# Optimization experiments

Hardware: AMD Instinct MI355X
Metric: run time of the kernel (lower is better)

Reference implementation:

```python
import jax, jax.numpy as jnp
import numpy as np

N_NODES = 100000
N_EDGES = 50000
NNZ = 400000          # 8 node slots per hyperedge, each node in exactly 4 hyperedges
IN_CH = 64            # ONE_HOT_0_ENCODING_SIZE
HID = 256
ALPHA = -1.5          # HNHN edge-cardinality exponent
BETA = -0.5           # HNHN node-cardinality exponent


def setup_inputs() -> dict:
    key = jax.random.key(0)
    ks = jax.random.split(key, 12)
    x_0 = jax.random.normal(ks[0], (N_NODES, IN_CH), dtype=jnp.float32)
    # COO incidence: every node appears NNZ//N_NODES times, every edge has NNZ//N_EDGES members
    rows = jax.random.permutation(
        ks[1], jnp.tile(jnp.arange(N_NODES, dtype=jnp.int32), NNZ // N_NODES))
    cols = jnp.repeat(jnp.arange(N_EDGES, dtype=jnp.int32), NNZ // N_EDGES)
    vals = jnp.ones((NNZ,), dtype=jnp.float32)

    def glorot(k, fi, fo):
        return jax.random.normal(k, (fi, fo), dtype=jnp.float32) * (2.0 / (fi + fo)) ** 0.5

    W0_l0 = glorot(ks[2], IN_CH, HID)
    W1_l0 = glorot(ks[3], HID, HID)
    W0_l1 = glorot(ks[4], HID, HID)
    W1_l1 = glorot(ks[5], HID, HID)
    b1_l0 = jax.random.normal(ks[6], (1, HID), dtype=jnp.float32) * 0.05
    b0_l0 = jax.random.normal(ks[7], (1, HID), dtype=jnp.float32) * 0.05
    b1_l1 = jax.random.normal(ks[8], (1, HID), dtype=jnp.float32) * 0.05
    b0_l1 = jax.random.normal(ks[9], (1, HID), dtype=jnp.float32) * 0.05
    lin_w = glorot(ks[10], HID, 1)
    lin_b = jnp.zeros((1,), dtype=jnp.float32)
    return dict(x_0=x_0, vals=vals, rows=rows, cols=cols,
                W0_l0=W0_l0, W1_l0=W1_l0, b1_l0=b1_l0, b0_l0=b0_l0,
                W0_l1=W0_l1, W1_l1=W1_l1, b1_l1=b1_l1, b0_l1=b0_l1,
                lin_w=lin_w, lin_b=lin_b)


def _normalized_vals(vals, rows, cols):
    """HNHN normalization of the incidence matrix B (n_nodes x n_edges).

    vals_n[k] : entry of  D0_left^{-1} B D1_right(|e|^alpha)        (edge->node)
    vals_t[k] : entry of (D1_left^{-1} B^T D0_right(d(v)^beta))^T   (node->edge)
    """
    seg = jax.ops.segment_sum
    edge_card = seg(vals, cols, num_segments=N_EDGES) ** ALPHA   # |e|^alpha
    node_card = seg(vals, rows, num_segments=N_NODES) ** BETA    # d(v)^beta
    nz = (vals != 0).astype(vals.dtype)                          # nonzero pattern
    d0_inv = 1.0 / seg(edge_card[cols] * nz, rows, num_segments=N_NODES)
    d1_inv = 1.0 / seg(node_card[rows] * nz, cols, num_segments=N_EDGES)
    vals_n = d0_inv[rows] * vals * edge_card[cols]
    vals_t = d1_inv[cols] * vals * node_card[rows]
    return vals_n, vals_t


def _hnhn_layer(x0, rows, cols, vals_n, vals_t, W0, W1, b1, b0):
    # node -> hyperedge: x_1 = relu(B_t_norm^T (x0 W0) + b1)
    m = (x0 @ W0)[rows] * vals_t[:, None]                 # [nnz, HID]
    x1 = jax.nn.relu(jax.ops.segment_sum(m, cols, num_segments=N_EDGES) + b1)
    # hyperedge -> node: x_0 = relu(B_norm (x1 W1) + b0)
    m = (x1 @ W1)[cols] * vals_n[:, None]                 # [nnz, HID]
    x0 = jax.nn.relu(jax.ops.segment_sum(m, rows, num_segments=N_NODES) + b0)
    return x0, x1


def reference(x_0, vals, rows, cols,
              W0_l0, W1_l0, b1_l0, b0_l0,
              W0_l1, W1_l1, b1_l1, b0_l1,
              lin_w, lin_b):
    vals_n, vals_t = _normalized_vals(vals, rows, cols)
    x0, _ = _hnhn_layer(x_0, rows, cols, vals_n, vals_t, W0_l0, W1_l0, b1_l0, b0_l0)
    x0, _ = _hnhn_layer(x0, rows, cols, vals_n, vals_t, W0_l1, W1_l1, b1_l1, b0_l1)
    pooled = jnp.max(x0, axis=0)                          # [HID]
    return pooled @ lin_w + lin_b                         # [1]
```

## Files before the change

kernel.cpp:

```cpp
#include <hip/hip_runtime.h>

#define N_NODES 100000
#define N_EDGES 50000
#define NNZ_    400000
#define MP 100032
#define EP 50048
#define NBN 98
#define NBE 49
#define PRED_ROWS 6250

typedef unsigned short ushort_t;
typedef unsigned int uint_t;

typedef __attribute__((ext_vector_type(8))) short bf16x8;
typedef __attribute__((ext_vector_type(4))) float f32x4;

__device__ __forceinline__ float b2f(ushort_t u) {
    return __uint_as_float(((uint_t)u) << 16);
}
__device__ __forceinline__ ushort_t f2b(float f) {
    uint_t x = __float_as_uint(f);
    uint_t r = (x + 0x7fffu + ((x >> 16) & 1u)) >> 16;
    return (ushort_t)r;
}
__device__ __forceinline__ float ldval(const void* p, int k, int bf) {
    return bf ? b2f(((const ushort_t*)p)[k]) : ((const float*)p)[k];
}
__device__ __forceinline__ float vb(bf16x8 v, int j) {
    return __uint_as_float(((uint_t)(ushort_t)v[j]) << 16);
}

__global__ void k_sentinel(void* out) { ((uint_t*)out)[0] = 0x44894489u; }

__global__ void k_zero(uint_t* p, size_t n) {
    size_t i = (size_t)blockIdx.x * 256 + threadIdx.x;
    size_t stride = (size_t)gridDim.x * 256;
    for (; i < n; i += stride) p[i] = 0u;
}

__global__ void k_checkfill(const void* __restrict__ vals, const int* __restrict__ rows,
                            const int* __restrict__ cols, int* ncntA, int* nidx,
                            int* flags) {
    int k = blockIdx.x * 256 + threadIdx.x;
    int bf = (((const uint_t*)vals)[0] == 0x3F803F80u);
    if (k == 0 && blockIdx.x == 0) flags[0] = bf;
    if (k >= NNZ_) return;
    int bad = 0;
    if (cols[k] != (k >> 3)) bad = 1;
    if (bf) { if (((const ushort_t*)vals)[k] != 0x3F80) bad = 1; }
    else    { if (((const uint_t*)vals)[k] != 0x3F800000u) bad = 1; }
    if (bad) atomicOr(&flags[2], 1);
    int r = rows[k];
    if ((unsigned)r >= (unsigned)N_NODES) { atomicOr(&flags[3], 1); return; }
    int slot = atomicAdd(&ncntA[r], 1);
    if (slot < 4) nidx[r * 4 + slot] = k;
    else atomicOr(&flags[3], 1);
}

__global__ void k_cvt_all(const void* x0, const void* W0l0, const void* W1l0,
                          const void* W0l1, const void* W1l1,
                          const void* b1l0, const void* b0l0, const void* b1l1,
                          const void* b0l1, const void* lw, const void* lb,
                          ushort_t* x0c, ushort_t* Wt0_l0, ushort_t* Wt1_l0,
                          ushort_t* Wt0_l1, ushort_t* Wt1_l1,
                          float* smallf, const int* __restrict__ flags) {
    int bf = flags[0];
    long i = (long)blockIdx.x * 256 + threadIdx.x;
    const long R0V = (long)N_NODES * 64 / 8;
    if (i < R0V) {
        if (!bf) {
            const float* s = (const float*)x0 + i * 8;
            bf16x8 o;
#pragma unroll
            for (int j = 0; j < 8; ++j) o[j] = (short)f2b(s[j]);
            *(bf16x8*)(x0c + i * 8) = o;
        }
        return;
    }
    i -= R0V;
    if (i < 64 * 256) {
        int kk = i >> 8, n = i & 255;
        Wt0_l0[n * 64 + kk] = bf ? ((const ushort_t*)W0l0)[i] : f2b(((const float*)W0l0)[i]);
        return;
    }
    i -= 64 * 256;
    if (i < 65536) {
        int kk = i >> 8, n = i & 255;
        Wt1_l0[n * 256 + kk] = bf ? ((const ushort_t*)W1l0)[i] : f2b(((const float*)W1l0)[i]);
        return;
    }
    i -= 65536;
    if (i < 65536) {
        int kk = i >> 8, n = i & 255;
        Wt0_l1[n * 256 + kk] = bf ? ((const ushort_t*)W0l1)[i] : f2b(((const float*)W0l1)[i]);
        return;
    }
    i -= 65536;
    if (i < 65536) {
        int kk = i >> 8, n = i & 255;
        Wt1_l1[n * 256 + kk] = bf ? ((const ushort_t*)W1l1)[i] : f2b(((const float*)W1l1)[i]);
        return;
    }
    i -= 65536;
    if (i < 1536) {
        int b = i >> 8, t = i & 255;
        const void* srcs[6] = {b1l0, b0l0, b1l1, b0l1, lw, lb};
        int sz = (b == 5) ? 1 : 256;
        if (t < sz) smallf[b * 256 + t] = ldval(srcs[b], t, bf);
    }
}

__global__ void k_hist(const void* __restrict__ vals, const int* __restrict__ rows,
                       const int* __restrict__ cols, int* node_cnt, int* edge_cnt,
                       float* node_delta, float* edge_delta, const int* __restrict__ flags) {
    if ((flags[2] | flags[3]) == 0) return;
    int k = blockIdx.x * 256 + threadIdx.x;
    if (k >= NNZ_) return;
    int r = rows[k], c = cols[k];
    atomicAdd(&node_cnt[r], 1);
    atomicAdd(&edge_cnt[c], 1);
    float v = ldval(vals, k, flags[0]);
    if (v != 1.0f) {
        atomicAdd(&node_delta[r], v - 1.0f);
        atomicAdd(&edge_delta[c], v - 1.0f);
    }
}

__global__ void k_pow(const int* node_cnt, const int* edge_cnt,
                      const float* node_delta, const float* edge_delta,
                      float* node_card, float* edge_card, const int* __restrict__ flags) {
    if ((flags[2] | flags[3]) == 0) return;
    int i = blockIdx.x * 256 + threadIdx.x;
    if (i < N_NODES) {
        float s = (float)node_cnt[i] + node_delta[i];
        node_card[i] = rsqrtf(s);
    }
    if (i < N_EDGES) {
        float s = (float)edge_cnt[i] + edge_delta[i];
        edge_card[i] = 1.0f / (s * sqrtf(s));
    }
}

__global__ void k_dsum(const void* __restrict__ vals, const int* __restrict__ rows,
                       const int* __restrict__ cols, const float* __restrict__ node_card,
                       const float* __restrict__ edge_card, float* d0, float* d1,
                       const int* __restrict__ flags) {
    if ((flags[2] | flags[3]) == 0) return;
    int t = blockIdx.x * 256 + threadIdx.x;
    if (flags[2] == 0) {
        if (t < N_EDGES) {
            const int* rp = rows + t * 8;
            float s = 0.f;
#pragma unroll
            for (int j = 0; j < 8; ++j) s += node_card[rp[j]];
            d1[t] = s;
        }
        if (t < N_NODES) d0[t] = (float)0;
    }
    if (t < NNZ_) {
        float v = ldval(vals, t, flags[0]);
        if (v != 0.0f) {
            int r = rows[t], c = cols[t];
            atomicAdd(&d0[r], edge_card[c]);
            if (flags[2] != 0) atomicAdd(&d1[c], node_card[r]);
        }
    }
}

__global__ void k_scan1(const int* __restrict__ ncnt, const int* __restrict__ ecnt,
                        int* __restrict__ nptr, int* __restrict__ eptr,
                        int* __restrict__ bsumN, int* __restrict__ bsumE,
                        const int* __restrict__ flags) {
    if ((flags[2] | flags[3]) == 0) return;
    __shared__ int s[256];
    int b = blockIdx.x;
    const int* cnt; int* ptr; int* bsum; int n;
    if (b < NBN) { cnt = ncnt; ptr = nptr; bsum = bsumN; n = N_NODES; }
    else { b -= NBN; cnt = ecnt; ptr = eptr; bsum = bsumE; n = N_EDGES; }
    int t = threadIdx.x;
    int base = b * 1024 + t * 4;
    int c0 = 0, c1 = 0, c2 = 0, c3 = 0;
    if (base + 0 < n) c0 = cnt[base + 0];
    if (base + 1 < n) c1 = cnt[base + 1];
    if (base + 2 < n) c2 = cnt[base + 2];
    if (base + 3 < n) c3 = cnt[base + 3];
    int s4 = c0 + c1 + c2 + c3;
    s[t] = s4;
    __syncthreads();
    for (int d = 1; d < 256; d <<= 1) {
        int v = (t >= d) ? s[t - d] : 0;
        __syncthreads();
        s[t] += v;
        __syncthreads();
    }
    int ex = s[t] - s4;
    if (base + 0 < n) ptr[base + 0] = ex;
    if (base + 1 < n) ptr[base + 1] = ex + c0;
    if (base + 2 < n) ptr[base + 2] = ex + c0 + c1;
    if (base + 3 < n) ptr[base + 3] = ex + c0 + c1 + c2;
    if (t == 255) bsum[b] = s[255];
}

__global__ void k_scan2(int* __restrict__ bsumN, int* __restrict__ bsumE,
                        int* __restrict__ nptr, int* __restrict__ eptr,
                        const int* __restrict__ flags) {
    if ((flags[2] | flags[3]) == 0) return;
    __shared__ int s[256];
    int* bsum; int nb; int* tot;
    if (blockIdx.x == 0) { bsum = bsumN; nb = NBN; tot = nptr + N_NODES; }
    else { bsum = bsumE; nb = NBE; tot = eptr + N_EDGES; }
    int t = threadIdx.x;
    int v = (t < nb) ? bsum[t] : 0;
    s[t] = v;
    __syncthreads();
    for (int d = 1; d < 256; d <<= 1) {
        int x = (t >= d) ? s[t - d] : 0;
        __syncthreads();
        s[t] += x;
        __syncthreads();
    }
    if (t < nb) bsum[t] = s[t] - v;
    if (t == 255) *tot = s[255];
}

__global__ void k_scan3(int* __restrict__ nptr, int* __restrict__ eptr,
                        const int* __restrict__ bsumN, const int* __restrict__ bsumE,
                        int* __restrict__ ncnt, int* __restrict__ ecnt,
                        int* __restrict__ ndeg, const int* __restrict__ flags) {
    if ((flags[2] | flags[3]) == 0) return;
    int b = blockIdx.x;
    if (b < 391) {
        int i = b * 256 + threadIdx.x;
        if (i < N_NODES) { nptr[i] += bsumN[i >> 10]; ndeg[i] = ncnt[i]; ncnt[i] = 0; }
    } else {
        int i = (b - 391) * 256 + threadIdx.x;
        if (i < N_EDGES) { eptr[i] += bsumE[i >> 10]; ecnt[i] = 0; }
    }
}

__global__ void k_fill(const int* __restrict__ rows, const int* __restrict__ cols,
                       const int* __restrict__ nptr, const int* __restrict__ eptr,
                       int* ncnt, int* ecnt, int* nidx, int* eidx,
                       const int* __restrict__ flags) {
    if ((flags[2] | flags[3]) == 0) return;
    int k = blockIdx.x * 256 + threadIdx.x;
    if (k >= NNZ_) return;
    int r = rows[k], c = cols[k];
    int pos = nptr[r] + atomicAdd(&ncnt[r], 1);
    nidx[pos] = k;
    int pe = eptr[c] + atomicAdd(&ecnt[c], 1);
    eidx[pe] = k;
}

__global__ void k_pairs(const void* __restrict__ vals, const int* __restrict__ rows,
                        const int* __restrict__ cols,
                        const int* __restrict__ nidx, const int* __restrict__ eidx,
                        const int* __restrict__ ndeg, const float* __restrict__ node_card,
                        const float* __restrict__ edge_card,
                        const float* __restrict__ d0, const float* __restrict__ d1,
                        int2* __restrict__ pairN, int2* __restrict__ pairE,
                        const int* __restrict__ flags) {
    if ((flags[2] | flags[3]) == 0) return;
    int i = blockIdx.x * 256 + threadIdx.x;
    if (i >= NNZ_) return;
    int bf = flags[0];
    int k = nidx[i];
    int r = rows[k], c = cols[k];
    float wn;
    if (flags[2] == 0) wn = (1.0f / (float)ndeg[r]);
    else               wn = ldval(vals, k, bf) * edge_card[c] / d0[r];
    pairN[i] = make_int2(c, __float_as_int(wn));
    int ke = eidx[i];
    int rr = rows[ke];
    float wt = ldval(vals, ke, bf) * node_card[rr] / d1[cols[ke]];
    pairE[i] = make_int2(rr, __float_as_int(wt));
}

template <int K>
__global__ __launch_bounds__(256) void k_gemm2(const ushort_t* __restrict__ A,
                                               const ushort_t* __restrict__ Wt,
                                               ushort_t* __restrict__ C,
                                               const float* __restrict__ bias,
                                               int do_relu) {
    __shared__ ushort_t lds[32 * 512];
    const int tid = threadIdx.x;
    const int lane = tid & 63;
    const int wave = tid >> 6;
    const int r16 = lane & 15;
    const int quad = lane >> 4;
    const int nh = blockIdx.x & 1;
    const int mblk = blockIdx.x >> 1;
    const int nbase = nh * 128;
    const int mbase = mblk * 64 + wave * 16;
    const ushort_t* Arow = A + (size_t)(mbase + r16) * K;

    f32x4 acc[8];
#pragma unroll
    for (int t = 0; t < 8; ++t) acc[t] = (f32x4){0.f, 0.f, 0.f, 0.f};

    constexpr int KCH = (K < 128) ? K : 128;
    constexpr int NF = (KCH / 32) * 8;
    for (int kc = 0; kc < K; kc += KCH) {
        __syncthreads();
        for (int f = wave; f < NF; f += 4) {
            int kb = f >> 3, t = f & 7;
            int n = nbase + t * 16 + r16;
            int kg = kc + kb * 32 + quad * 8;
            *(bf16x8*)(&lds[f * 512 + lane * 8]) = *(const bf16x8*)(Wt + (size_t)n * K + kg);
        }
        __syncthreads();
#pragma unroll
        for (int k0 = 0; k0 < KCH; k0 += 32) {
            bf16x8 af = *(const bf16x8*)(Arow + kc + k0 + quad * 8);
#pragma unroll
            for (int t = 0; t < 8; ++t) {
                bf16x8 bfr = *(const bf16x8*)(&lds[((k0 >> 5) * 8 + t) * 512 + lane * 8]);
                acc[t] = __builtin_amdgcn_mfma_f32_16x16x32_bf16(af, bfr, acc[t], 0, 0, 0);
            }
        }
    }
    const int mo = mbase + quad * 4;
#pragma unroll
    for (int t = 0; t < 8; ++t) {
        int n = nbase + t * 16 + r16;
        float b = bias ? bias[n] : 0.f;
#pragma unroll
        for (int r = 0; r < 4; ++r) {
            float v = acc[t][r] + b;
            if (do_relu) v = fmaxf(v, 0.f);
            C[(size_t)(mo + r) * 256 + n] = f2b(v);
        }
    }
}

template <int C>
__global__ __launch_bounds__(256) void k_aggE(const ushort_t* __restrict__ srcA,
                                              const ushort_t* __restrict__ srcB,
                                              const int* __restrict__ rows,
                                              const int* __restrict__ eptr,
                                              const int2* __restrict__ pairE,
                                              ushort_t* __restrict__ dst,
                                              const int* __restrict__ flags) {
    constexpr int TPS = C / 8;
    constexpr int SPB = 256 / TPS;
    const int sub = threadIdx.x / TPS;
    const int ch8 = (threadIdx.x % TPS) * 8;
    const int segA = blockIdx.x * (2 * SPB) + sub;
    const int segB = segA + SPB;
    const ushort_t* src = flags[0] ? srcA : srcB;
    const int sA = min(segA, N_EDGES - 1), sB = min(segB, N_EDGES - 1);
    float accA[8], accB[8];
    if ((flags[2] | flags[3]) == 0) {
        int4 a0 = *(const int4*)(rows + sA * 8);
        int4 a1 = *(const int4*)(rows + sA * 8 + 4);
        int4 b0 = *(const int4*)(rows + sB * 8);
        int4 b1 = *(const int4*)(rows + sB * 8 + 4);
        bf16x8 va0 = *(const bf16x8*)(src + (size_t)a0.x * C + ch8);
        bf16x8 va1 = *(const bf16x8*)(src + (size_t)a0.y * C + ch8);
        bf16x8 va2 = *(const bf16x8*)(src + (size_t)a0.z * C + ch8);
        bf16x8 va3 = *(const bf16x8*)(src + (size_t)a0.w * C + ch8);
        bf16x8 va4 = *(const bf16x8*)(src + (size_t)a1.x * C + ch8);
        bf16x8 va5 = *(const bf16x8*)(src + (size_t)a1.y * C + ch8);
        bf16x8 va6 = *(const bf16x8*)(src + (size_t)a1.z * C + ch8);
        bf16x8 va7 = *(const bf16x8*)(src + (size_t)a1.w * C + ch8);
        bf16x8 vb0 = *(const bf16x8*)(src + (size_t)b0.x * C + ch8);
        bf16x8 vb1 = *(const bf16x8*)(src + (size_t)b0.y * C + ch8);
        bf16x8 vb2 = *(const bf16x8*)(src + (size_t)b0.z * C + ch8);
        bf16x8 vb3 = *(const bf16x8*)(src + (size_t)b0.w * C + ch8);
        bf16x8 vb4 = *(const bf16x8*)(src + (size_t)b1.x * C + ch8);
        bf16x8 vb5 = *(const bf16x8*)(src + (size_t)b1.y * C + ch8);
        bf16x8 vb6 = *(const bf16x8*)(src + (size_t)b1.z * C + ch8);
        bf16x8 vb7 = *(const bf16x8*)(src + (size_t)b1.w * C + ch8);
#pragma unroll
        for (int j = 0; j < 8; ++j) {
            accA[j] = 0.125f * (((vb(va0,j) + vb(va1,j)) + (vb(va2,j) + vb(va3,j))) +
                                ((vb(va4,j) + vb(va5,j)) + (vb(va6,j) + vb(va7,j))));
            accB[j] = 0.125f * (((vb(vb0,j) + vb(vb1,j)) + (vb(vb2,j) + vb(vb3,j))) +
                                ((vb(vb4,j) + vb(vb5,j)) + (vb(vb6,j) + vb(vb7,j))));
        }
    } else {
        float* accs[2] = {accA, accB};
        int segs[2] = {sA, sB};
        for (int p = 0; p < 2; ++p) {
            float* a = accs[p];
#pragma unroll
            for (int j = 0; j < 8; ++j) a[j] = 0.f;
            int lo = eptr[segs[p]], hi = eptr[segs[p] + 1];
            for (int i = lo; i < hi; ++i) {
                int2 pr = pairE[i];
                float w = __int_as_float(pr.y);
                bf16x8 v = *(const bf16x8*)(src + (size_t)pr.x * C + ch8);
#pragma unroll
                for (int j = 0; j < 8; ++j) a[j] += w * vb(v, j);
            }
        }
    }
    bf16x8 oA, oB;
#pragma unroll
    for (int j = 0; j < 8; ++j) { oA[j] = (short)f2b(accA[j]); oB[j] = (short)f2b(accB[j]); }
    if (segA < N_EDGES) *(bf16x8*)(dst + (size_t)segA * C + ch8) = oA;
    if (segB < N_EDGES) *(bf16x8*)(dst + (size_t)segB * C + ch8) = oB;
}

template <int POOL>
__global__ __launch_bounds__(256) void k_aggN(const ushort_t* __restrict__ src,
                                              const int* __restrict__ nidx,
                                              const int* __restrict__ nptr,
                                              const int2* __restrict__ pairN,
                                              const float* __restrict__ bias,
                                              ushort_t* __restrict__ dst,
                                              float* __restrict__ partial,
                                              const int* __restrict__ flags) {
    __shared__ float sm[8][256];
    const int tid = threadIdx.x;
    const int sub = tid >> 5;
    const int ch8 = (tid & 31) * 8;
    const int segA = blockIdx.x * 16 + sub;
    const int segB = segA + 8;
    float accA[8], accB[8];
    if ((flags[2] | flags[3]) == 0) {
        int4 iA = *(const int4*)(nidx + segA * 4);
        int4 iB = *(const int4*)(nidx + segB * 4);
        bf16x8 vA0 = *(const bf16x8*)(src + (size_t)(iA.x >> 3) * 256 + ch8);
        bf16x8 vA1 = *(const bf16x8*)(src + (size_t)(iA.y >> 3) * 256 + ch8);
        bf16x8 vA2 = *(const bf16x8*)(src + (size_t)(iA.z >> 3) * 256 + ch8);
        bf16x8 vA3 = *(const bf16x8*)(src + (size_t)(iA.w >> 3) * 256 + ch8);
        bf16x8 vB0 = *(const bf16x8*)(src + (size_t)(iB.x >> 3) * 256 + ch8);
        bf16x8 vB1 = *(const bf16x8*)(src + (size_t)(iB.y >> 3) * 256 + ch8);
        bf16x8 vB2 = *(const bf16x8*)(src + (size_t)(iB.z >> 3) * 256 + ch8);
        bf16x8 vB3 = *(const bf16x8*)(src + (size_t)(iB.w >> 3) * 256 + ch8);
#pragma unroll
        for (int j = 0; j < 8; ++j) {
            accA[j] = 0.25f * ((vb(vA0,j) + vb(vA1,j)) + (vb(vA2,j) + vb(vA3,j)));
            accB[j] = 0.25f * ((vb(vB0,j) + vb(vB1,j)) + (vb(vB2,j) + vb(vB3,j)));
        }
    } else {
        float* accs[2] = {accA, accB};
        int segs[2] = {segA, segB};
        for (int p = 0; p < 2; ++p) {
            float* a = accs[p];
#pragma unroll
            for (int j = 0; j < 8; ++j) a[j] = 0.f;
            int lo = nptr[segs[p]], hi = nptr[segs[p] + 1];
            for (int i = lo; i < hi; ++i) {
                int2 pr = pairN[i];
                float w = __int_as_float(pr.y);
                bf16x8 v = *(const bf16x8*)(src + (size_t)pr.x * 256 + ch8);
#pragma unroll
                for (int j = 0; j < 8; ++j) a[j] += w * vb(v, j);
            }
        }
    }
    if (POOL) {
#pragma unroll
        for (int j = 0; j < 8; ++j) {
            float rA = fmaxf(accA[j] + bias[ch8 + j], 0.f);
            float rB = fmaxf(accB[j] + bias[ch8 + j], 0.f);
            sm[sub][ch8 + j] = fmaxf(rA, rB);
        }
        __syncthreads();
        float mm = sm[0][tid];
#pragma unroll
        for (int g = 1; g < 8; ++g) mm = fmaxf(mm, sm[g][tid]);
        partial[(size_t)blockIdx.x * 256 + tid] = mm;
    } else {
        bf16x8 oA, oB;
#pragma unroll
        for (int j = 0; j < 8; ++j) {
            oA[j] = (short)f2b(fmaxf(accA[j] + bias[ch8 + j], 0.f));
            oB[j] = (short)f2b(fmaxf(accB[j] + bias[ch8 + j], 0.f));
        }
        *(bf16x8*)(dst + (size_t)segA * 256 + ch8) = oA;
        *(bf16x8*)(dst + (size_t)segB * 256 + ch8) = oB;
    }
}

__global__ void k_pred(const float* __restrict__ partial, float* pooled) {
    int ch = threadIdx.x;
    float m = 0.f;
    for (int r = blockIdx.x; r < PRED_ROWS; r += gridDim.x)
        m = fmaxf(m, partial[(size_t)r * 256 + ch]);
    atomicMax((int*)&pooled[ch], __float_as_int(m));
}

__global__ void k_final(const float* __restrict__ pooled, const float* __restrict__ smallf,
                        void* out, const int* __restrict__ flags) {
    __shared__ float red[256];
    int c = threadIdx.x;
    red[c] = pooled[c] * smallf[4 * 256 + c];
    __syncthreads();
    for (int s = 128; s > 0; s >>= 1) {
        if (c < s) red[c] += red[c + s];
        __syncthreads();
    }
    if (c == 0) {
        float r = red[0] + smallf[5 * 256 + 0];
        if (flags[0]) ((ushort_t*)out)[0] = f2b(r);
        else          ((float*)out)[0] = r;
    }
}

extern "C" void kernel_launch(void* const* d_in, const int* in_sizes, int n_in,
                              void* d_out, int out_size, void* d_ws, size_t ws_size,
                              hipStream_t stream) {
    const void* x0_in = d_in[0];
    const void* vals  = d_in[1];
    const int* rows = (const int*)d_in[2];
    const int* cols = (const int*)d_in[3];
    const void* W0_l0 = d_in[4];
    const void* W1_l0 = d_in[5];
    const void* b1_l0 = d_in[6];
    const void* b0_l0 = d_in[7];
    const void* W0_l1 = d_in[8];
    const void* W1_l1 = d_in[9];
    const void* b1_l1 = d_in[10];
    const void* b0_l1 = d_in[11];
    const void* lin_w = d_in[12];
    const void* lin_b = d_in[13];

    char* ws = (char*)d_ws;
    size_t off = 0;
    auto alloc = [&](size_t bytes) { size_t o = off; off += (bytes + 255) & ~(size_t)255; return o; };

    size_t o_ncntA      = alloc(MP * 4);
    size_t o_node_cnt   = alloc(MP * 4);
    size_t o_edge_cnt   = alloc(EP * 4);
    size_t o_node_delta = alloc(MP * 4);
    size_t o_edge_delta = alloc(EP * 4);
    size_t o_d0         = alloc(MP * 4);
    size_t o_d1         = alloc(EP * 4);
    size_t o_pooled     = alloc(256 * 4);
    size_t o_flags      = alloc(256);
    size_t zero_end     = off;
    size_t o_ndeg      = alloc(MP * 4);
    size_t o_node_card = alloc(MP * 4);
    size_t o_edge_card = alloc(EP * 4);
    size_t o_node_ptr = alloc((size_t)(MP + 1) * 4);
    size_t o_edge_ptr = alloc((size_t)(EP + 1) * 4);
    size_t o_node_idx = alloc((size_t)NNZ_ * 4);
    size_t o_edge_idx = alloc((size_t)NNZ_ * 4);
    size_t o_bsumN    = alloc(512);
    size_t o_bsumE    = alloc(512);
    size_t o_smallf   = alloc(6 * 256 * 4);
    size_t o_pairN    = alloc((size_t)NNZ_ * 8);
    size_t o_pairE    = alloc((size_t)NNZ_ * 8);
    size_t o_Wt0_l0 = alloc(256 * 64 * 2);
    size_t o_Wt1_l0 = alloc(256 * 256 * 2);
    size_t o_Wt0_l1 = alloc(256 * 256 * 2);
    size_t o_Wt1_l1 = alloc(256 * 256 * 2);
    size_t o_E1 = alloc((size_t)EP * 256 * 2);
    size_t o_E2 = alloc((size_t)EP * 256 * 2);
    size_t o_N1 = alloc((size_t)MP * 256 * 2);
    if (off > ws_size) {
        k_sentinel<<<1, 1, 0, stream>>>(d_out);
        return;
    }

    int* ncntA = (int*)(ws + o_ncntA);
    int* node_cnt = (int*)(ws + o_node_cnt);
    int* edge_cnt = (int*)(ws + o_edge_cnt);
    float* node_delta = (float*)(ws + o_node_delta);
    float* edge_delta = (float*)(ws + o_edge_delta);
    float* d0 = (float*)(ws + o_d0);
    float* d1 = (float*)(ws + o_d1);
    float* pooled = (float*)(ws + o_pooled);
    int* flags = (int*)(ws + o_flags);
    int* ndeg = (int*)(ws + o_ndeg);
    float* node_card = (float*)(ws + o_node_card);
    float* edge_card = (float*)(ws + o_edge_card);
    int* node_ptr = (int*)(ws + o_node_ptr);
    int* edge_ptr = (int*)(ws + o_edge_ptr);
    int* node_idx = (int*)(ws + o_node_idx);
    int* edge_idx = (int*)(ws + o_edge_idx);
    int* bsumN = (int*)(ws + o_bsumN);
    int* bsumE = (int*)(ws + o_bsumE);
    float* smallf = (float*)(ws + o_smallf);
    int2* pairN = (int2*)(ws + o_pairN);
    int2* pairE = (int2*)(ws + o_pairE);
    ushort_t* Wt0_l0 = (ushort_t*)(ws + o_Wt0_l0);
    ushort_t* Wt1_l0 = (ushort_t*)(ws + o_Wt1_l0);
    ushort_t* Wt0_l1 = (ushort_t*)(ws + o_Wt0_l1);
    ushort_t* Wt1_l1 = (ushort_t*)(ws + o_Wt1_l1);
    ushort_t* E1 = (ushort_t*)(ws + o_E1);
    ushort_t* E2 = (ushort_t*)(ws + o_E2);
    ushort_t* N1 = (ushort_t*)(ws + o_N1);
    float* partial = (float*)(ws + o_E2);
    ushort_t* x0c = (ushort_t*)(ws + o_E2);

    const int NB = (NNZ_ + 255) / 256;
    const int CVB = 3964;
    const int GB = (EP / 64) * 2;

    k_zero<<<512, 256, 0, stream>>>((uint_t*)ws, zero_end / 4);
    k_checkfill<<<NB, 256, 0, stream>>>(vals, rows, cols, ncntA, node_idx, flags);
    k_cvt_all<<<CVB, 256, 0, stream>>>(x0_in, W0_l0, W1_l0, W0_l1, W1_l1,
                                       b1_l0, b0_l0, b1_l1, b0_l1, lin_w, lin_b,
                                       x0c, Wt0_l0, Wt1_l0, Wt0_l1, Wt1_l1, smallf, flags);

    k_hist<<<NB, 256, 0, stream>>>(vals, rows, cols, node_cnt, edge_cnt,
                                   node_delta, edge_delta, flags);
    k_pow<<<(N_NODES + 255) / 256, 256, 0, stream>>>(node_cnt, edge_cnt, node_delta,
                                                     edge_delta, node_card, edge_card, flags);
    k_dsum<<<NB, 256, 0, stream>>>(vals, rows, cols, node_card, edge_card, d0, d1, flags);
    k_scan1<<<NBN + NBE, 256, 0, stream>>>(node_cnt, edge_cnt, node_ptr, edge_ptr,
                                           bsumN, bsumE, flags);
    k_scan2<<<2, 256, 0, stream>>>(bsumN, bsumE, node_ptr, edge_ptr, flags);
    k_scan3<<<391 + 196, 256, 0, stream>>>(node_ptr, edge_ptr, bsumN, bsumE,
                                           node_cnt, edge_cnt, ndeg, flags);
    k_fill<<<NB, 256, 0, stream>>>(rows, cols, node_ptr, edge_ptr, node_cnt, edge_cnt,
                                   node_idx, edge_idx, flags);
    k_pairs<<<NB, 256, 0, stream>>>(vals, rows, cols, node_idx, edge_idx, ndeg,
                                    node_card, edge_card, d0, d1, pairN, pairE, flags);

    k_aggE<64><<<(N_EDGES + 63) / 64, 256, 0, stream>>>((const ushort_t*)x0_in, x0c, rows,
                                                        edge_ptr, pairE, E1, flags);
    k_gemm2<64><<<GB, 256, 0, stream>>>(E1, Wt0_l0, E2, smallf + 0 * 256, 1);
    k_gemm2<256><<<GB, 256, 0, stream>>>(E2, Wt1_l0, E1, nullptr, 0);
    k_aggN<0><<<N_NODES / 16, 256, 0, stream>>>(E1, node_idx, node_ptr, pairN,
                                                smallf + 1 * 256, N1, nullptr, flags);

    k_aggE<256><<<(N_EDGES + 15) / 16, 256, 0, stream>>>(N1, N1, rows, edge_ptr, pairE,
                                                         E1, flags);
    k_gemm2<256><<<GB, 256, 0, stream>>>(E1, Wt0_l1, E2, smallf + 2 * 256, 1);
    k_gemm2<256><<<GB, 256, 0, stream>>>(E2, Wt1_l1, E1, nullptr, 0);
    k_aggN<1><<<N_NODES / 16, 256, 0, stream>>>(E1, node_idx, node_ptr, pairN,
                                                smallf + 3 * 256, nullptr, partial, flags);

    k_pred<<<64, 256, 0, stream>>>(partial, pooled);
    k_final<<<1, 256, 0, stream>>>(pooled, smallf, d_out, flags);
}
```

Baseline: 361.4 us.

## Panelize aggregation kernels by channel slice and merge prep kernels into one

The node and edge aggregation kernels now split channels into narrow panels, with each block covering one channel slice across many segments. Each gather then touches a smaller band of feature columns, which should improve cache reuse. The fallback preprocessing (histogram, power, degree sums, scans, fill, pairs) is merged into one single-block kernel, removing several launches. The fast path's node index list now stores edge ids directly. The risks are narrow 16/32-channel gathers with poor sector utilisation and a very slow fallback path on one workgroup.

```diff
diff --git a/kernel.cpp b/kernel.cpp
--- a/kernel.cpp
+++ b/kernel.cpp
@@ -5,9 +5,8 @@
 #define NNZ_    400000
 #define MP 100032
 #define EP 50048
-#define NBN 98
-#define NBE 49
-#define PRED_ROWS 6250
+#define NBLK_N 1563
+#define NBLK_E 391
 
 typedef unsigned short ushort_t;
 typedef unsigned int uint_t;
@@ -53,7 +52,7 @@
     int r = rows[k];
     if ((unsigned)r >= (unsigned)N_NODES) { atomicOr(&flags[3], 1); return; }
     int slot = atomicAdd(&ncntA[r], 1);
-    if (slot < 4) nidx[r * 4 + slot] = k;
+    if (slot < 4) nidx[r * 4 + slot] = (k >> 3);
     else atomicOr(&flags[3], 1);
 }
 
@@ -110,170 +109,98 @@
     }
 }
 
-__global__ void k_hist(const void* __restrict__ vals, const int* __restrict__ rows,
-                       const int* __restrict__ cols, int* node_cnt, int* edge_cnt,
-                       float* node_delta, float* edge_delta, const int* __restrict__ flags) {
+__global__ __launch_bounds__(1024) void k_genprep(
+        const void* __restrict__ vals, const int* __restrict__ rows,
+        const int* __restrict__ cols, int* ncnt, int* ecnt,
+        float* ndelta, float* edelta, float* ncard, float* ecard,
+        float* d0, float* d1, int* nptr, int* eptr, int* nidx, int* eidx,
+        int2* pairN, int2* pairE, const int* __restrict__ flags) {
     if ((flags[2] | flags[3]) == 0) return;
-    int k = blockIdx.x * 256 + threadIdx.x;
-    if (k >= NNZ_) return;
-    int r = rows[k], c = cols[k];
-    atomicAdd(&node_cnt[r], 1);
-    atomicAdd(&edge_cnt[c], 1);
-    float v = ldval(vals, k, flags[0]);
-    if (v != 1.0f) {
-        atomicAdd(&node_delta[r], v - 1.0f);
-        atomicAdd(&edge_delta[c], v - 1.0f);
-    }
-}
-
-__global__ void k_pow(const int* node_cnt, const int* edge_cnt,
-                      const float* node_delta, const float* edge_delta,
-                      float* node_card, float* edge_card, const int* __restrict__ flags) {
-    if ((flags[2] | flags[3]) == 0) return;
-    int i = blockIdx.x * 256 + threadIdx.x;
-    if (i < N_NODES) {
-        float s = (float)node_cnt[i] + node_delta[i];
-        node_card[i] = rsqrtf(s);
-    }
-    if (i < N_EDGES) {
-        float s = (float)edge_cnt[i] + edge_delta[i];
-        edge_card[i] = 1.0f / (s * sqrtf(s));
-    }
-}
-
-__global__ void k_dsum(const void* __restrict__ vals, const int* __restrict__ rows,
-                       const int* __restrict__ cols, const float* __restrict__ node_card,
-                       const float* __restrict__ edge_card, float* d0, float* d1,
-                       const int* __restrict__ flags) {
-    if ((flags[2] | flags[3]) == 0) return;
-    int t = blockIdx.x * 256 + threadIdx.x;
-    if (flags[2] == 0) {
-        if (t < N_EDGES) {
-            const int* rp = rows + t * 8;
-            float s = 0.f;
-#pragma unroll
-            for (int j = 0; j < 8; ++j) s += node_card[rp[j]];
-            d1[t] = s;
-        }
-        if (t < N_NODES) d0[t] = (float)0;
-    }
-    if (t < NNZ_) {
-        float v = ldval(vals, t, flags[0]);
-        if (v != 0.0f) {
-            int r = rows[t], c = cols[t];
-            atomicAdd(&d0[r], edge_card[c]);
-            if (flags[2] != 0) atomicAdd(&d1[c], node_card[r]);
-        }
-    }
-}
-
-__global__ void k_scan1(const int* __restrict__ ncnt, const int* __restrict__ ecnt,
-                        int* __restrict__ nptr, int* __restrict__ eptr,
-                        int* __restrict__ bsumN, int* __restrict__ bsumE,
-                        const int* __restrict__ flags) {
-    if ((flags[2] | flags[3]) == 0) return;
-    __shared__ int s[256];
-    int b = blockIdx.x;
-    const int* cnt; int* ptr; int* bsum; int n;
-    if (b < NBN) { cnt = ncnt; ptr = nptr; bsum = bsumN; n = N_NODES; }
-    else { b -= NBN; cnt = ecnt; ptr = eptr; bsum = bsumE; n = N_EDGES; }
+    __shared__ int ss[1024];
     int t = threadIdx.x;
-    int base = b * 1024 + t * 4;
-    int c0 = 0, c1 = 0, c2 = 0, c3 = 0;
-    if (base + 0 < n) c0 = cnt[base + 0];
-    if (base + 1 < n) c1 = cnt[base + 1];
-    if (base + 2 < n) c2 = cnt[base + 2];
-    if (base + 3 < n) c3 = cnt[base + 3];
-    int s4 = c0 + c1 + c2 + c3;
-    s[t] = s4;
-    __syncthreads();
-    for (int d = 1; d < 256; d <<= 1) {
-        int v = (t >= d) ? s[t - d] : 0;
-        __syncthreads();
-        s[t] += v;
-        __syncthreads();
-    }
-    int ex = s[t] - s4;
-    if (base + 0 < n) ptr[base + 0] = ex;
-    if (base + 1 < n) ptr[base + 1] = ex + c0;
-    if (base + 2 < n) ptr[base + 2] = ex + c0 + c1;
-    if (base + 3 < n) ptr[base + 3] = ex + c0 + c1 + c2;
-    if (t == 255) bsum[b] = s[255];
-}
-
-__global__ void k_scan2(int* __restrict__ bsumN, int* __restrict__ bsumE,
-                        int* __restrict__ nptr, int* __restrict__ eptr,
-                        const int* __restrict__ flags) {
-    if ((flags[2] | flags[3]) == 0) return;
-    __shared__ int s[256];
-    int* bsum; int nb; int* tot;
-    if (blockIdx.x == 0) { bsum = bsumN; nb = NBN; tot = nptr + N_NODES; }
-    else { bsum = bsumE; nb = NBE; tot = eptr + N_EDGES; }
-    int t = threadIdx.x;
-    int v = (t < nb) ? bsum[t] : 0;
-    s[t] = v;
-    __syncthreads();
-    for (int d = 1; d < 256; d <<= 1) {
-        int x = (t >= d) ? s[t - d] : 0;
-        __syncthreads();
-        s[t] += x;
-        __syncthreads();
-    }
-    if (t < nb) bsum[t] = s[t] - v;
-    if (t == 255) *tot = s[255];
-}
-
-__global__ void k_scan3(int* __restrict__ nptr, int* __restrict__ eptr,
-                        const int* __restrict__ bsumN, const int* __restrict__ bsumE,
-                        int* __restrict__ ncnt, int* __restrict__ ecnt,
-                        int* __restrict__ ndeg, const int* __restrict__ flags) {
-    if ((flags[2] | flags[3]) == 0) return;
-    int b = blockIdx.x;
-    if (b < 391) {
-        int i = b * 256 + threadIdx.x;
-        if (i < N_NODES) { nptr[i] += bsumN[i >> 10]; ndeg[i] = ncnt[i]; ncnt[i] = 0; }
-    } else {
-        int i = (b - 391) * 256 + threadIdx.x;
-        if (i < N_EDGES) { eptr[i] += bsumE[i >> 10]; ecnt[i] = 0; }
-    }
-}
-
-__global__ void k_fill(const int* __restrict__ rows, const int* __restrict__ cols,
-                       const int* __restrict__ nptr, const int* __restrict__ eptr,
-                       int* ncnt, int* ecnt, int* nidx, int* eidx,
-                       const int* __restrict__ flags) {
-    if ((flags[2] | flags[3]) == 0) return;
-    int k = blockIdx.x * 256 + threadIdx.x;
-    if (k >= NNZ_) return;
-    int r = rows[k], c = cols[k];
-    int pos = nptr[r] + atomicAdd(&ncnt[r], 1);
-    nidx[pos] = k;
-    int pe = eptr[c] + atomicAdd(&ecnt[c], 1);
-    eidx[pe] = k;
-}
-
-__global__ void k_pairs(const void* __restrict__ vals, const int* __restrict__ rows,
-                        const int* __restrict__ cols,
-                        const int* __restrict__ nidx, const int* __restrict__ eidx,
-                        const int* __restrict__ ndeg, const float* __restrict__ node_card,
-                        const float* __restrict__ edge_card,
-                        const float* __restrict__ d0, const float* __restrict__ d1,
-                        int2* __restrict__ pairN, int2* __restrict__ pairE,
-                        const int* __restrict__ flags) {
-    if ((flags[2] | flags[3]) == 0) return;
-    int i = blockIdx.x * 256 + threadIdx.x;
-    if (i >= NNZ_) return;
     int bf = flags[0];
-    int k = nidx[i];
-    int r = rows[k], c = cols[k];
-    float wn;
-    if (flags[2] == 0) wn = (1.0f / (float)ndeg[r]);
-    else               wn = ldval(vals, k, bf) * edge_card[c] / d0[r];
-    pairN[i] = make_int2(c, __float_as_int(wn));
-    int ke = eidx[i];
-    int rr = rows[ke];
-    float wt = ldval(vals, ke, bf) * node_card[rr] / d1[cols[ke]];
-    pairE[i] = make_int2(rr, __float_as_int(wt));
+    for (int i = t; i < MP; i += 1024) { ncnt[i] = 0; ndelta[i] = 0.f; d0[i] = 0.f; }
+    for (int i = t; i < EP; i += 1024) { ecnt[i] = 0; edelta[i] = 0.f; d1[i] = 0.f; }
+    __syncthreads();
+    for (int k = t; k < NNZ_; k += 1024) {
+        int r = rows[k], c = cols[k];
+        if ((unsigned)r < (unsigned)N_NODES) atomicAdd(&ncnt[r], 1);
+        if ((unsigned)c < (unsigned)N_EDGES) atomicAdd(&ecnt[c], 1);
+        float v = ldval(vals, k, bf);
+        if (v != 1.0f && (unsigned)r < (unsigned)N_NODES && (unsigned)c < (unsigned)N_EDGES) {
+            atomicAdd(&ndelta[r], v - 1.f); atomicAdd(&edelta[c], v - 1.f);
+        }
+    }
+    __syncthreads();
+    for (int i = t; i < N_NODES; i += 1024) ncard[i] = rsqrtf((float)ncnt[i] + ndelta[i]);
+    for (int i = t; i < N_EDGES; i += 1024) {
+        float s = (float)ecnt[i] + edelta[i];
+        ecard[i] = 1.f / (s * sqrtf(s));
+    }
+    __syncthreads();
+    for (int k = t; k < NNZ_; k += 1024) {
+        int r = rows[k], c = cols[k];
+        if ((unsigned)r >= (unsigned)N_NODES || (unsigned)c >= (unsigned)N_EDGES) continue;
+        float v = ldval(vals, k, bf);
+        if (v != 0.f) {
+            atomicAdd(&d0[r], ecard[c]); atomicAdd(&d1[c], ncard[r]);
+        }
+    }
+    __syncthreads();
+    {
+        int chunk = (N_NODES + 1023) / 1024;
+        int lo = t * chunk, hi = min(lo + chunk, N_NODES);
+        int s = 0;
+        for (int i = lo; i < hi; ++i) s += ncnt[i];
+        ss[t] = s; __syncthreads();
+        if (t == 0) {
+            int acc = 0;
+            for (int i = 0; i < 1024; ++i) { int x = ss[i]; ss[i] = acc; acc += x; }
+            nptr[N_NODES] = acc;
+        }
+        __syncthreads();
+        int acc = ss[t];
+        for (int i = lo; i < hi; ++i) { nptr[i] = acc; acc += ncnt[i]; }
+        __syncthreads();
+        chunk = (N_EDGES + 1023) / 1024;
+        lo = t * chunk; hi = min(lo + chunk, N_EDGES);
+        s = 0;
+        for (int i = lo; i < hi; ++i) s += ecnt[i];
+        ss[t] = s; __syncthreads();
+        if (t == 0) {
+            int acc2 = 0;
+            for (int i = 0; i < 1024; ++i) { int x = ss[i]; ss[i] = acc2; acc2 += x; }
+            eptr[N_EDGES] = acc2;
+        }
+        __syncthreads();
+        acc = ss[t];
+        for (int i = lo; i < hi; ++i) { eptr[i] = acc; acc += ecnt[i]; }
+        __syncthreads();
+    }
+    for (int i = t; i < N_NODES; i += 1024) ncnt[i] = 0;
+    for (int i = t; i < N_EDGES; i += 1024) ecnt[i] = 0;
+    __syncthreads();
+    for (int k = t; k < NNZ_; k += 1024) {
+        int r = rows[k], c = cols[k];
+        if ((unsigned)r >= (unsigned)N_NODES || (unsigned)c >= (unsigned)N_EDGES) continue;
+        nidx[nptr[r] + atomicAdd(&ncnt[r], 1)] = k;
+        eidx[eptr[c] + atomicAdd(&ecnt[c], 1)] = k;
+    }
+    __syncthreads();
+    int tot = nptr[N_NODES];
+    for (int i = t; i < tot; i += 1024) {
+        int k = nidx[i];
+        int r = rows[k], c = cols[k];
+        float wn = ldval(vals, k, bf) * ecard[c] / d0[r];
+        pairN[i] = make_int2(c, __float_as_int(wn));
+    }
+    int tote = eptr[N_EDGES];
+    for (int i = t; i < tote; i += 1024) {
+        int ke = eidx[i];
+        int rr = rows[ke];
+        float wt = ldval(vals, ke, bf) * ncard[rr] / d1[cols[ke]];
+        pairE[i] = make_int2(rr, __float_as_int(wt));
+    }
 }
 
 template <int K>
@@ -334,152 +261,125 @@
 }
 
 template <int C>
-__global__ __launch_bounds__(256) void k_aggE(const ushort_t* __restrict__ srcA,
-                                              const ushort_t* __restrict__ srcB,
-                                              const int* __restrict__ rows,
-                                              const int* __restrict__ eptr,
-                                              const int2* __restrict__ pairE,
-                                              ushort_t* __restrict__ dst,
-                                              const int* __restrict__ flags) {
-    constexpr int TPS = C / 8;
-    constexpr int SPB = 256 / TPS;
-    const int sub = threadIdx.x / TPS;
-    const int ch8 = (threadIdx.x % TPS) * 8;
-    const int segA = blockIdx.x * (2 * SPB) + sub;
-    const int segB = segA + SPB;
+__global__ __launch_bounds__(256) void k_aggEp(const ushort_t* __restrict__ srcA,
+                                               const ushort_t* __restrict__ srcB,
+                                               const int* __restrict__ rows,
+                                               const int* __restrict__ eptr,
+                                               const int2* __restrict__ pairE,
+                                               ushort_t* __restrict__ dst,
+                                               const int* __restrict__ flags) {
+    const int panel = blockIdx.x / NBLK_E;
+    const int blk = blockIdx.x % NBLK_E;
+    const int sub = threadIdx.x >> 1;
+    const int ch = panel * 16 + (threadIdx.x & 1) * 8;
+    const int seg = blk * 128 + sub;
+    if (seg >= N_EDGES) return;
     const ushort_t* src = flags[0] ? srcA : srcB;
-    const int sA = min(segA, N_EDGES - 1), sB = min(segB, N_EDGES - 1);
-    float accA[8], accB[8];
+    float acc[8];
     if ((flags[2] | flags[3]) == 0) {
-        int4 a0 = *(const int4*)(rows + sA * 8);
-        int4 a1 = *(const int4*)(rows + sA * 8 + 4);
-        int4 b0 = *(const int4*)(rows + sB * 8);
-        int4 b1 = *(const int4*)(rows + sB * 8 + 4);
-        bf16x8 va0 = *(const bf16x8*)(src + (size_t)a0.x * C + ch8);
-        bf16x8 va1 = *(const bf16x8*)(src + (size_t)a0.y * C + ch8);
-        bf16x8 va2 = *(const bf16x8*)(src + (size_t)a0.z * C + ch8);
-        bf16x8 va3 = *(const bf16x8*)(src + (size_t)a0.w * C + ch8);
-        bf16x8 va4 = *(const bf16x8*)(src + (size_t)a1.x * C + ch8);
-        bf16x8 va5 = *(const bf16x8*)(src + (size_t)a1.y * C + ch8);
-        bf16x8 va6 = *(const bf16x8*)(src + (size_t)a1.z * C + ch8);
-        bf16x8 va7 = *(const bf16x8*)(src + (size_t)a1.w * C + ch8);
-        bf16x8 vb0 = *(const bf16x8*)(src + (size_t)b0.x * C + ch8);
-        bf16x8 vb1 = *(const bf16x8*)(src + (size_t)b0.y * C + ch8);
-        bf16x8 vb2 = *(const bf16x8*)(src + (size_t)b0.z * C + ch8);
-        bf16x8 vb3 = *(const bf16x8*)(src + (size_t)b0.w * C + ch8);
-        bf16x8 vb4 = *(const bf16x8*)(src + (size_t)b1.x * C + ch8);
-        bf16x8 vb5 = *(const bf16x8*)(src + (size_t)b1.y * C + ch8);
-        bf16x8 vb6 = *(const bf16x8*)(src + (size_t)b1.z * C + ch8);
-        bf16x8 vb7 = *(const bf16x8*)(src + (size_t)b1.w * C + ch8);
-#pragma unroll
-        for (int j = 0; j < 8; ++j) {
-            accA[j] = 0.125f * (((vb(va0,j) + vb(va1,j)) + (vb(va2,j) + vb(va3,j))) +
-                                ((vb(va4,j) + vb(va5,j)) + (vb(va6,j) + vb(va7,j))));
-            accB[j] = 0.125f * (((vb(vb0,j) + vb(vb1,j)) + (vb(vb2,j) + vb(vb3,j))) +
-                                ((vb(vb4,j) + vb(vb5,j)) + (vb(vb6,j) + vb(vb7,j))));
-        }
+        int4 a0 = *(const int4*)(rows + seg * 8);
+        int4 a1 = *(const int4*)(rows + seg * 8 + 4);
+        bf16x8 v0 = *(const bf16x8*)(src + (size_t)a0.x * C + ch);
+        bf16x8 v1 = *(const bf16x8*)(src + (size_t)a0.y * C + ch);
+        bf16x8 v2 = *(const bf16x8*)(src + (size_t)a0.z * C + ch);
+        bf16x8 v3 = *(const bf16x8*)(src + (size_t)a0.w * C + ch);
+        bf16x8 v4 = *(const bf16x8*)(src + (size_t)a1.x * C + ch);
+        bf16x8 v5 = *(const bf16x8*)(src + (size_t)a1.y * C + ch);
+        bf16x8 v6 = *(const bf16x8*)(src + (size_t)a1.z * C + ch);
+        bf16x8 v7 = *(const bf16x8*)(src + (size_t)a1.w * C + ch);
+#pragma unroll
+        for (int j = 0; j < 8; ++j)
+            acc[j] = 0.125f * (((vb(v0,j) + vb(v1,j)) + (vb(v2,j) + vb(v3,j))) +
+                               ((vb(v4,j) + vb(v5,j)) + (vb(v6,j) + vb(v7,j))));
     } else {
-        float* accs[2] = {accA, accB};
-        int segs[2] = {sA, sB};
-        for (int p = 0; p < 2; ++p) {
-            float* a = accs[p];
-#pragma unroll
-            for (int j = 0; j < 8; ++j) a[j] = 0.f;
-            int lo = eptr[segs[p]], hi = eptr[segs[p] + 1];
-            for (int i = lo; i < hi; ++i) {
-                int2 pr = pairE[i];
-                float w = __int_as_float(pr.y);
-                bf16x8 v = *(const bf16x8*)(src + (size_t)pr.x * C + ch8);
-#pragma unroll
-                for (int j = 0; j < 8; ++j) a[j] += w * vb(v, j);
-            }
-        }
-    }
-    bf16x8 oA, oB;
-#pragma unroll
-    for (int j = 0; j < 8; ++j) { oA[j] = (short)f2b(accA[j]); oB[j] = (short)f2b(accB[j]); }
-    if (segA < N_EDGES) *(bf16x8*)(dst + (size_t)segA * C + ch8) = oA;
-    if (segB < N_EDGES) *(bf16x8*)(dst + (size_t)segB * C + ch8) = oB;
+#pragma unroll
+        for (int j = 0; j < 8; ++j) acc[j] = 0.f;
+        int lo = eptr[seg], hi = eptr[seg + 1];
+        for (int i = lo; i < hi; ++i) {
+            int2 pr = pairE[i];
+            float w = __int_as_float(pr.y);
+            bf16x8 v = *(const bf16x8*)(src + (size_t)pr.x * C + ch);
+#pragma unroll
+            for (int j = 0; j < 8; ++j) acc[j] += w * vb(v, j);
+        }
+    }
+    bf16x8 o;
+#pragma unroll
+    for (int j = 0; j < 8; ++j) o[j] = (short)f2b(acc[j]);
+    *(bf16x8*)(dst + (size_t)seg * C + ch) = o;
 }
 
 template <int POOL>
-__global__ __launch_bounds__(256) void k_aggN(const ushort_t* __restrict__ src,
-                                              const int* __restrict__ nidx,
-                                              const int* __restrict__ nptr,
-                                              const int2* __restrict__ pairN,
-                                              const float* __restrict__ bias,
-                                              ushort_t* __restrict__ dst,
-                                              float* __restrict__ partial,
-                                              const int* __restrict__ flags) {
-    __shared__ float sm[8][256];
-    const int tid = threadIdx.x;
-    const int sub = tid >> 5;
-    const int ch8 = (tid & 31) * 8;
-    const int segA = blockIdx.x * 16 + sub;
-    const int segB = segA + 8;
-    float accA[8], accB[8];
-    if ((flags[2] | flags[3]) == 0) {
-        int4 iA = *(const int4*)(nidx + segA * 4);
-        int4 iB = *(const int4*)(nidx + segB * 4);
-        bf16x8 vA0 = *(const bf16x8*)(src + (size_t)(iA.x >> 3) * 256 + ch8);
-        bf16x8 vA1 = *(const bf16x8*)(src + (size_t)(iA.y >> 3) * 256 + ch8);
-        bf16x8 vA2 = *(const bf16x8*)(src + (size_t)(iA.z >> 3) * 256 + ch8);
-        bf16x8 vA3 = *(const bf16x8*)(src + (size_t)(iA.w >> 3) * 256 + ch8);
-        bf16x8 vB0 = *(const bf16x8*)(src + (size_t)(iB.x >> 3) * 256 + ch8);
-        bf16x8 vB1 = *(const bf16x8*)(src + (size_t)(iB.y >> 3) * 256 + ch8);
-        bf16x8 vB2 = *(const bf16x8*)(src + (size_t)(iB.z >> 3) * 256 + ch8);
-        bf16x8 vB3 = *(const bf16x8*)(src + (size_t)(iB.w >> 3) * 256 + ch8);
-#pragma unroll
-        for (int j = 0; j < 8; ++j) {
-            accA[j] = 0.25f * ((vb(vA0,j) + vb(vA1,j)) + (vb(vA2,j) + vb(vA3,j)));
-            accB[j] = 0.25f * ((vb(vB0,j) + vb(vB1,j)) + (vb(vB2,j) + vb(vB3,j)));
-        }
-    } else {
-        float* accs[2] = {accA, accB};
-        int segs[2] = {segA, segB};
-        for (int p = 0; p < 2; ++p) {
-            float* a = accs[p];
-#pragma unroll
-            for (int j = 0; j < 8; ++j) a[j] = 0.f;
-            int lo = nptr[segs[p]], hi = nptr[segs[p] + 1];
+__global__ __launch_bounds__(256) void k_aggNp(const ushort_t* __restrict__ src,
+                                               const int* __restrict__ nidx,
+                                               const int* __restrict__ nptr,
+                                               const int2* __restrict__ pairN,
+                                               const float* __restrict__ bias,
+                                               ushort_t* __restrict__ dst,
+                                               float* __restrict__ partial,
+                                               const int* __restrict__ flags) {
+    __shared__ float sm[64][33];
+    const int panel = blockIdx.x / NBLK_N;
+    const int blk = blockIdx.x % NBLK_N;
+    const int sub = threadIdx.x >> 2;
+    const int chp = (threadIdx.x & 3) * 8;
+    const int ch = panel * 32 + chp;
+    const int seg = blk * 64 + sub;
+    const int valid = (seg < N_NODES);
+    if (!POOL && !valid) return;
+    float acc[8];
+    if (valid) {
+        if ((flags[2] | flags[3]) == 0) {
+            int4 i4 = *(const int4*)(nidx + seg * 4);
+            bf16x8 v0 = *(const bf16x8*)(src + (size_t)i4.x * 256 + ch);
+            bf16x8 v1 = *(const bf16x8*)(src + (size_t)i4.y * 256 + ch);
+            bf16x8 v2 = *(const bf16x8*)(src + (size_t)i4.z * 256 + ch);
+            bf16x8 v3 = *(const bf16x8*)(src + (size_t)i4.w * 256 + ch);
+#pragma unroll
+            for (int j = 0; j < 8; ++j)
+                acc[j] = 0.25f * ((vb(v0,j) + vb(v1,j)) + (vb(v2,j) + vb(v3,j)));
+        } else {
+#pragma unroll
+            for (int j = 0; j < 8; ++j) acc[j] = 0.f;
+            int lo = nptr[seg], hi = nptr[seg + 1];
             for (int i = lo; i < hi; ++i) {
                 int2 pr = pairN[i];
                 float w = __int_as_float(pr.y);
-                bf16x8 v = *(const bf16x8*)(src + (size_t)pr.x * 256 + ch8);
-#pragma unroll
-                for (int j = 0; j < 8; ++j) a[j] += w * vb(v, j);
+                bf16x8 v = *(const bf16x8*)(src + (size_t)pr.x * 256 + ch);
+#pragma unroll
+                for (int j = 0; j < 8; ++j) acc[j] += w * vb(v, j);
             }
         }
+    } else {
+#pragma unroll
+        for (int j = 0; j < 8; ++j) acc[j] = 0.f;
     }
     if (POOL) {
 #pragma unroll
-        for (int j = 0; j < 8; ++j) {
-            float rA = fmaxf(accA[j] + bias[ch8 + j], 0.f);
-            float rB = fmaxf(accB[j] + bias[ch8 + j], 0.f);
-            sm[sub][ch8 + j] = fmaxf(rA, rB);
-        }
-        __syncthreads();
-        float mm = sm[0][tid];
-#pragma unroll
-        for (int g = 1; g < 8; ++g) mm = fmaxf(mm, sm[g][tid]);
-        partial[(size_t)blockIdx.x * 256 + tid] = mm;
+        for (int j = 0; j < 8; ++j)
+            sm[sub][chp + j] = valid ? fmaxf(acc[j] + bias[ch + j], 0.f) : 0.f;
+        __syncthreads();
+        if (threadIdx.x < 32) {
+            float m = sm[0][threadIdx.x];
+#pragma unroll 8
+            for (int g = 1; g < 64; ++g) m = fmaxf(m, sm[g][threadIdx.x]);
+            partial[(size_t)blockIdx.x * 32 + threadIdx.x] = m;
+        }
     } else {
-        bf16x8 oA, oB;
-#pragma unroll
-        for (int j = 0; j < 8; ++j) {
-            oA[j] = (short)f2b(fmaxf(accA[j] + bias[ch8 + j], 0.f));
-            oB[j] = (short)f2b(fmaxf(accB[j] + bias[ch8 + j], 0.f));
-        }
-        *(bf16x8*)(dst + (size_t)segA * 256 + ch8) = oA;
-        *(bf16x8*)(dst + (size_t)segB * 256 + ch8) = oB;
+        bf16x8 o;
+#pragma unroll
+        for (int j = 0; j < 8; ++j)
+            o[j] = (short)f2b(fmaxf(acc[j] + bias[ch + j], 0.f));
+        *(bf16x8*)(dst + (size_t)seg * 256 + ch) = o;
     }
 }
 
 __global__ void k_pred(const float* __restrict__ partial, float* pooled) {
     int ch = threadIdx.x;
+    int panel = ch >> 5, i = ch & 31;
     float m = 0.f;
-    for (int r = blockIdx.x; r < PRED_ROWS; r += gridDim.x)
-        m = fmaxf(m, partial[(size_t)r * 256 + ch]);
+    for (int b = blockIdx.x; b < NBLK_N; b += gridDim.x)
+        m = fmaxf(m, partial[(size_t)(panel * NBLK_N + b) * 32 + i]);
     atomicMax((int*)&pooled[ch], __float_as_int(m));
 }
 
@@ -522,25 +422,22 @@
     size_t off = 0;
     auto alloc = [&](size_t bytes) { size_t o = off; off += (bytes + 255) & ~(size_t)255; return o; };
 
-    size_t o_ncntA      = alloc(MP * 4);
+    size_t o_ncntA  = alloc(MP * 4);
+    size_t o_pooled = alloc(256 * 4);
+    size_t o_flags  = alloc(256);
+    size_t zero_end = off;
     size_t o_node_cnt   = alloc(MP * 4);
     size_t o_edge_cnt   = alloc(EP * 4);
     size_t o_node_delta = alloc(MP * 4);
     size_t o_edge_delta = alloc(EP * 4);
     size_t o_d0         = alloc(MP * 4);
     size_t o_d1         = alloc(EP * 4);
-    size_t o_pooled     = alloc(256 * 4);
-    size_t o_flags      = alloc(256);
-    size_t zero_end     = off;
-    size_t o_ndeg      = alloc(MP * 4);
     size_t o_node_card = alloc(MP * 4);
     size_t o_edge_card = alloc(EP * 4);
     size_t o_node_ptr = alloc((size_t)(MP + 1) * 4);
     size_t o_edge_ptr = alloc((size_t)(EP + 1) * 4);
     size_t o_node_idx = alloc((size_t)NNZ_ * 4);
     size_t o_edge_idx = alloc((size_t)NNZ_ * 4);
-    size_t o_bsumN    = alloc(512);
-    size_t o_bsumE    = alloc(512);
     size_t o_smallf   = alloc(6 * 256 * 4);
     size_t o_pairN    = alloc((size_t)NNZ_ * 8);
     size_t o_pairE    = alloc((size_t)NNZ_ * 8);
@@ -557,23 +454,20 @@
     }
 
     int* ncntA = (int*)(ws + o_ncntA);
+    float* pooled = (float*)(ws + o_pooled);
+    int* flags = (int*)(ws + o_flags);
     int* node_cnt = (int*)(ws + o_node_cnt);
     int* edge_cnt = (int*)(ws + o_edge_cnt);
     float* node_delta = (float*)(ws + o_node_delta);
     float* edge_delta = (float*)(ws + o_edge_delta);
     float* d0 = (float*)(ws + o_d0);
     float* d1 = (float*)(ws + o_d1);
-    float* pooled = (float*)(ws + o_pooled);
-    int* flags = (int*)(ws + o_flags);
-    int* ndeg = (int*)(ws + o_ndeg);
     float* node_card = (float*)(ws + o_node_card);
     float* edge_card = (float*)(ws + o_edge_card);
     int* node_ptr = (int*)(ws + o_node_ptr);
     int* edge_ptr = (int*)(ws + o_edge_ptr);
     int* node_idx = (int*)(ws + o_node_idx);
     int* edge_idx = (int*)(ws + o_edge_idx);
-    int* bsumN = (int*)(ws + o_bsumN);
-    int* bsumE = (int*)(ws + o_bsumE);
     float* smallf = (float*)(ws + o_smallf);
     int2* pairN = (int2*)(ws + o_pairN);
     int2* pairE = (int2*)(ws + o_pairE);
@@ -591,40 +485,29 @@
     const int CVB = 3964;
     const int GB = (EP / 64) * 2;
 
-    k_zero<<<512, 256, 0, stream>>>((uint_t*)ws, zero_end / 4);
+    k_zero<<<128, 256, 0, stream>>>((uint_t*)ws, zero_end / 4);
     k_checkfill<<<NB, 256, 0, stream>>>(vals, rows, cols, ncntA, node_idx, flags);
     k_cvt_all<<<CVB, 256, 0, stream>>>(x0_in, W0_l0, W1_l0, W0_l1, W1_l1,
                                        b1_l0, b0_l0, b1_l1, b0_l1, lin_w, lin_b,
                                        x0c, Wt0_l0, Wt1_l0, Wt0_l1, Wt1_l1, smallf, flags);
-
-    k_hist<<<NB, 256, 0, stream>>>(vals, rows, cols, node_cnt, edge_cnt,
-                                   node_delta, edge_delta, flags);
-    k_pow<<<(N_NODES + 255) / 256, 256, 0, stream>>>(node_cnt, edge_cnt, node_delta,
-                                                     edge_delta, node_card, edge_card, flags);
-    k_dsum<<<NB, 256, 0, stream>>>(vals, rows, cols, node_card, edge_card, d0, d1, flags);
-    k_scan1<<<NBN + NBE, 256, 0, stream>>>(node_cnt, edge_cnt, node_ptr, edge_ptr,
-                                           bsumN, bsumE, flags);
-    k_scan2<<<2, 256, 0, stream>>>(bsumN, bsumE, node_ptr, edge_ptr, flags);
-    k_scan3<<<391 + 196, 256, 0, stream>>>(node_ptr, edge_ptr, bsumN, bsumE,
-                                           node_cnt, edge_cnt, ndeg, flags);
-    k_fill<<<NB, 256, 0, stream>>>(rows, cols, node_ptr, edge_ptr, node_cnt, edge_cnt,
-                                   node_idx, edge_idx, flags);
-    k_pairs<<<NB, 256, 0, stream>>>(vals, rows, cols, node_idx, edge_idx, ndeg,
-                                    node_card, edge_card, d0, d1, pairN, pairE, flags);
-
-    k_aggE<64><<<(N_EDGES + 63) / 64, 256, 0, stream>>>((const ushort_t*)x0_in, x0c, rows,
-                                                        edge_ptr, pairE, E1, flags);
+    k_genprep<<<1, 1024, 0, stream>>>(vals, rows, cols, node_cnt, edge_cnt,
+                                      node_delta, edge_delta, node_card, edge_card,
+                                      d0, d1, node_ptr, edge_ptr, node_idx, edge_idx,
+                                      pairN, pairE, flags);
+
+    k_aggEp<64><<<NBLK_E * 4, 256, 0, stream>>>((const ushort_t*)x0_in, x0c, rows,
+                                                edge_ptr, pairE, E1, flags);
     k_gemm2<64><<<GB, 256, 0, stream>>>(E1, Wt0_l0, E2, smallf + 0 * 256, 1);
     k_gemm2<256><<<GB, 256, 0, stream>>>(E2, Wt1_l0, E1, nullptr, 0);
-    k_aggN<0><<<N_NODES / 16, 256, 0, stream>>>(E1, node_idx, node_ptr, pairN,
-                                                smallf + 1 * 256, N1, nullptr, flags);
-
-    k_aggE<256><<<(N_EDGES + 15) / 16, 256, 0, stream>>>(N1, N1, rows, edge_ptr, pairE,
-                                                         E1, flags);
+    k_aggNp<0><<<NBLK_N * 8, 256, 0, stream>>>(E1, node_idx, node_ptr, pairN,
+                                               smallf + 1 * 256, N1, nullptr, flags);
+
+    k_aggEp<256><<<NBLK_E * 16, 256, 0, stream>>>(N1, N1, rows, edge_ptr, pairE,
+                                                  E1, flags);
     k_gemm2<256><<<GB, 256, 0, stream>>>(E1, Wt0_l1, E2, smallf + 2 * 256, 1);
     k_gemm2<256><<<GB, 256, 0, stream>>>(E2, Wt1_l1, E1, nullptr, 0);
-    k_aggN<1><<<N_NODES / 16, 256, 0, stream>>>(E1, node_idx, node_ptr, pairN,
-                                                smallf + 3 * 256, nullptr, partial, flags);
+    k_aggNp<1><<<NBLK_N * 8, 256, 0, stream>>>(E1, node_idx, node_ptr, pairN,
+                                               smallf + 3 * 256, nullptr, partial, flags);
 
     k_pred<<<64, 256, 0, stream>>>(partial, pooled);
     k_final<<<1, 256, 0, stream>>>(pooled, smallf, d_out, flags);
```

Result: slower. 450.5 us (+24.6%).
